# Performance work log

Hardware: AMD Instinct MI355X
Metric: run time of the kernel (lower is better)

## Reference

```python
import jax, jax.numpy as jnp
import numpy as np

N_NODES = 50000
N_EDGES = 800000
NEG_SLOPE = 0.2  # PyG GATConv default


def _glorot(key, shape):
    fan_in = shape[0] if len(shape) > 1 else shape[0]
    return jax.random.normal(key, shape, dtype=jnp.float32) / jnp.sqrt(jnp.float32(fan_in))


def setup_inputs() -> dict:
    key = jax.random.key(0)
    ks = jax.random.split(key, 12)
    x = jax.random.normal(ks[0], (N_NODES, 128), dtype=jnp.float32)
    edge_index = jax.random.randint(ks[1], (2, N_EDGES), 0, N_NODES, dtype=jnp.int64)
    return {
        "x": x,
        "edge_index": edge_index,
        # GAT layer 1: 128 -> 128 (heads=1)
        "W1": _glorot(ks[2], (128, 128)),
        "a_src1": _glorot(ks[3], (128,)),
        "a_dst1": _glorot(ks[4], (128,)),
        "b1": jnp.zeros((128,), dtype=jnp.float32),
        "Wres1": _glorot(ks[5], (128, 128)),
        # GAT layer 2: 128 -> 256
        "W2": _glorot(ks[6], (128, 256)),
        "a_src2": _glorot(ks[7], (256,)),
        "a_dst2": _glorot(ks[8], (256,)),
        "b2": jnp.zeros((256,), dtype=jnp.float32),
        "Wres2": _glorot(ks[9], (128, 256)),
    }


def _gat_layer(x, src, dst, W, a_src, a_dst, b, Wres, n):
    # h: [N, C_out] transformed node features
    h = x @ W
    # per-edge attention logit: gather scalar contributions, LeakyReLU
    logit = jax.nn.leaky_relu((h @ a_src)[src] + (h @ a_dst)[dst], NEG_SLOPE)  # [E]
    # numerically stable segment softmax over incoming edges of each dst node
    seg_max = jax.ops.segment_max(logit, dst, num_segments=n)  # [N]
    ex = jnp.exp(logit - seg_max[dst])
    denom = jax.ops.segment_sum(ex, dst, num_segments=n)  # [N]
    alpha = ex / denom[dst]  # [E]; self-loops guarantee denom > 0
    # weighted scatter-add aggregation
    out = jax.ops.segment_sum(alpha[:, None] * h[src], dst, num_segments=n)  # [N, C_out]
    # residual projection (in_dim != out_dim) + bias
    return out + x @ Wres + b


def reference(x, edge_index, W1, a_src1, a_dst1, b1, Wres1, W2, a_src2, a_dst2, b2, Wres2):
    n = x.shape[0]
    loops = jnp.arange(n, dtype=edge_index.dtype)  # add_self_loops=True (PyG default)
    src = jnp.concatenate([edge_index[0], loops])
    dst = jnp.concatenate([edge_index[1], loops])
    h = _gat_layer(x, src, dst, W1, a_src1, a_dst1, b1, Wres1, n)
    h = jax.nn.relu(h)
    return _gat_layer(h, src, dst, W2, a_src2, a_dst2, b2, Wres2, n)
```

## Files before the change

### kernel.cpp

```cpp
#include <hip/hip_runtime.h>
#include <math.h>

typedef __attribute__((ext_vector_type(8))) short bf16x8;
typedef __attribute__((ext_vector_type(4))) float f32x4;

__device__ inline unsigned short f2bf(float f) {
  union { float f; unsigned u; } x; x.f = f;
  unsigned r = x.u + 0x7FFF + ((x.u >> 16) & 1);
  return (unsigned short)(r >> 16);
}
__device__ inline float bf2f(unsigned short b) {
  union { unsigned u; float f; } x; x.u = ((unsigned)b) << 16;
  return x.f;
}


__global__ void convert_kernel(const void* edges, int E, int N,
                               int* __restrict__ src32, int* __restrict__ dst32,
                               int* __restrict__ counts) {
  int i = blockIdx.x * blockDim.x + threadIdx.x;
  int tot = E + N;
  if (i >= tot) return;
  int s, d;
  if (i < E) {
    const long long* q = (const long long*)edges;
    bool i64 = true;
#pragma unroll
    for (int k = 0; k < 8; ++k) {
      long long v = q[k];
      if (v < 0 || v >= (long long)N) i64 = false;
    }
    if (i64) {
      s = (int)q[i];
      d = (int)q[E + i];
    } else {
      s = ((const int*)edges)[i];
      d = ((const int*)edges)[E + i];
    }
  } else {
    s = d = i - E;
  }
  src32[i] = s;
  dst32[i] = d;
  atomicAdd(&counts[d], 1);
}


__global__ __launch_bounds__(256) void scan_partial(const int* __restrict__ counts,
                                                    int* __restrict__ bsum, int n) {
  int t = threadIdx.x;
  int base = blockIdx.x * 1024 + t * 4;
  int s = 0;
#pragma unroll
  for (int k = 0; k < 4; ++k) {
    int i = base + k;
    if (i < n) s += counts[i];
  }
#pragma unroll
  for (int off = 32; off; off >>= 1) s += __shfl_xor(s, off);
  __shared__ int red[4];
  if ((t & 63) == 0) red[t >> 6] = s;
  __syncthreads();
  if (t == 0) bsum[blockIdx.x] = red[0] + red[1] + red[2] + red[3];
}

__global__ __launch_bounds__(256) void scan_bsum(const int* __restrict__ bsum,
                                                 int* __restrict__ ebsum,
                                                 int* __restrict__ rowptr, int nblk, int n) {
  __shared__ int sh[256];
  int t = threadIdx.x;
  int v = (t < nblk) ? bsum[t] : 0;
  sh[t] = v;
  __syncthreads();
  for (int off = 1; off < 256; off <<= 1) {
    int u = (t >= off) ? sh[t - off] : 0;
    __syncthreads();
    sh[t] += u;
    __syncthreads();
  }
  if (t < nblk) ebsum[t] = sh[t] - v;
  if (t == nblk - 1) rowptr[n] = sh[t];
}

__global__ __launch_bounds__(256) void scan_final(const int* __restrict__ counts,
                                                  const int* __restrict__ ebsum,
                                                  int* __restrict__ rowptr,
                                                  int* __restrict__ cursor, int n) {
  int t = threadIdx.x;
  int lane = t & 63;
  int wv = t >> 6;
  int base = blockIdx.x * 1024 + t * 4;
  int c[4];
  int ts = 0;
#pragma unroll
  for (int k = 0; k < 4; ++k) {
    int i = base + k;
    c[k] = (i < n) ? counts[i] : 0;
    ts += c[k];
  }
  int ws = ts;
  for (int off = 1; off < 64; off <<= 1) {
    int u = __shfl_up(ws, off);
    if (lane >= off) ws += u;
  }
  __shared__ int wtot[4];
  if (lane == 63) wtot[wv] = ws;
  __syncthreads();
  int woff = 0;
  for (int k = 0; k < 4; ++k)
    if (k < wv) woff += wtot[k];
  int run = ebsum[blockIdx.x] + woff + (ws - ts);
#pragma unroll
  for (int k = 0; k < 4; ++k) {
    int i = base + k;
    if (i < n) {
      rowptr[i] = run;
      cursor[i] = run;
    }
    run += c[k];
  }
}

__global__ void scatter_kernel(const int* __restrict__ src32, const int* __restrict__ dst32,
                               int* __restrict__ cursor, int* __restrict__ csr_src, int tot) {
  int i = blockIdx.x * blockDim.x + threadIdx.x;
  if (i >= tot) return;
  int d = dst32[i];
  int slot = atomicAdd(&cursor[d], 1);
  csr_src[slot] = src32[i];
}


__global__ void cvt_all(const float* __restrict__ x,
                        const float* __restrict__ W1, const float* __restrict__ Wres1,
                        const float* __restrict__ W2, const float* __restrict__ Wres2,
                        unsigned short* __restrict__ x16,
                        unsigned short* __restrict__ w1t, unsigned short* __restrict__ wres1t,
                        unsigned short* __restrict__ w2t, unsigned short* __restrict__ wres2t,
                        int N, int Mpad) {
  int tid = blockIdx.x * blockDim.x + threadIdx.x;
  int xcnt = Mpad * 32;
  if (tid < xcnt) {
    int row = tid >> 5;
    int q = (tid & 31) << 2;
    unsigned short o0 = 0, o1 = 0, o2 = 0, o3 = 0;
    if (row < N) {
      float4 v = *(const float4*)(x + (size_t)row * 128 + q);
      o0 = f2bf(v.x); o1 = f2bf(v.y); o2 = f2bf(v.z); o3 = f2bf(v.w);
    }
    unsigned short* p = x16 + (size_t)row * 128 + q;
    p[0] = o0; p[1] = o1; p[2] = o2; p[3] = o3;
    return;
  }
  int t2 = tid - xcnt;
  const float* W;
  unsigned short* Wt;
  int C, loc;
  if (t2 < 16384) { W = W1; Wt = w1t; C = 128; loc = t2; }
  else if (t2 < 32768) { W = Wres1; Wt = wres1t; C = 128; loc = t2 - 16384; }
  else if (t2 < 65536) { W = W2; Wt = w2t; C = 256; loc = t2 - 32768; }
  else if (t2 < 98304) { W = Wres2; Wt = wres2t; C = 256; loc = t2 - 65536; }
  else return;
  int c = loc >> 7;
  int k = loc & 127;
  Wt[(size_t)c * 128 + k] = f2bf(W[(size_t)k * C + c]);
}


__global__ __launch_bounds__(256) void gemm_dual(
    const unsigned short* __restrict__ A,
    const unsigned short* __restrict__ Bh, const unsigned short* __restrict__ Br,
    unsigned short* __restrict__ Hout, unsigned short* __restrict__ Rout,
    const float* __restrict__ bias,
    const float* __restrict__ a_src, const float* __restrict__ a_dst,
    float* __restrict__ as_, float* __restrict__ ad_,
    int Nrows, int Ctot) {
  int l = threadIdx.x & 63;
  int w = threadIdx.x >> 6;
  int row_w = blockIdx.x * 128 + (w & 1) * 64;
  int col_w = blockIdx.y * 128 + (w >> 1) * 64;
  int lo = l & 15, hi = l >> 4;
  f32x4 ah[4][4], ar[4][4];
#pragma unroll
  for (int i = 0; i < 4; ++i)
#pragma unroll
    for (int j = 0; j < 4; ++j) {
      ah[i][j] = (f32x4){0.f, 0.f, 0.f, 0.f};
      ar[i][j] = (f32x4){0.f, 0.f, 0.f, 0.f};
    }

  const unsigned short* Ap = A + (size_t)(row_w + lo) * 128 + hi * 8;
  const unsigned short* Bhp = Bh + (size_t)(col_w + lo) * 128 + hi * 8;
  const unsigned short* Brp = Br + (size_t)(col_w + lo) * 128 + hi * 8;
#pragma unroll
  for (int kk = 0; kk < 4; ++kk) {
    bf16x8 a[4], bh[4], br[4];
#pragma unroll
    for (int f = 0; f < 4; ++f) {
      a[f] = *(const bf16x8*)(Ap + (size_t)f * 16 * 128 + kk * 32);
      bh[f] = *(const bf16x8*)(Bhp + (size_t)f * 16 * 128 + kk * 32);
      br[f] = *(const bf16x8*)(Brp + (size_t)f * 16 * 128 + kk * 32);
    }
#pragma unroll
    for (int fr = 0; fr < 4; ++fr)
#pragma unroll
      for (int fc = 0; fc < 4; ++fc) {
        ah[fr][fc] = __builtin_amdgcn_mfma_f32_16x16x32_bf16(a[fr], bh[fc], ah[fr][fc], 0, 0, 0);
        ar[fr][fc] = __builtin_amdgcn_mfma_f32_16x16x32_bf16(a[fr], br[fc], ar[fr][fc], 0, 0, 0);
      }
  }
  float wsrc[4], wdst[4], wb[4];
#pragma unroll
  for (int fc = 0; fc < 4; ++fc) {
    int col = col_w + fc * 16 + lo;
    wsrc[fc] = a_src[col];
    wdst[fc] = a_dst[col];
    wb[fc] = bias[col];
  }
#pragma unroll
  for (int fr = 0; fr < 4; ++fr) {
#pragma unroll
    for (int r = 0; r < 4; ++r) {
      int row = row_w + fr * 16 + hi * 4 + r;
      if (row < Nrows) {
        float s1 = 0.f, s2 = 0.f;
#pragma unroll
        for (int fc = 0; fc < 4; ++fc) {
          int col = col_w + fc * 16 + lo;
          float vh = ah[fr][fc][r];
          Hout[(size_t)row * Ctot + col] = f2bf(vh);
          s1 = fmaf(vh, wsrc[fc], s1);
          s2 = fmaf(vh, wdst[fc], s2);
          Rout[(size_t)row * Ctot + col] = f2bf(ar[fr][fc][r] + wb[fc]);
        }
#pragma unroll
        for (int off = 8; off; off >>= 1) {
          s1 += __shfl_xor(s1, off);
          s2 += __shfl_xor(s2, off);
        }
        if (lo == 0) {
          atomicAdd(&as_[row], s1);
          atomicAdd(&ad_[row], s2);
        }
      }
    }
  }
}


template <int C, bool L1>
__global__ __launch_bounds__(256) void aggregate_kernel(
    const unsigned short* __restrict__ h, unsigned short* __restrict__ res,
    float* __restrict__ outf,
    const float* __restrict__ as_, const float* __restrict__ ad_,
    const int* __restrict__ rowptr, const int* __restrict__ csr_src, int N) {
  const int FPL = C / 64;
  int wid = blockIdx.x * 4 + (threadIdx.x >> 6);
  int lane = threadIdx.x & 63;
  if (wid >= N) return;
  int base = rowptr[wid];
  int deg = rowptr[wid + 1] - base;
  float adn = ad_[wid];
  float m = -1e30f, ssum = 0.f;
  float acc[FPL];
#pragma unroll
  for (int c = 0; c < FPL; ++c) acc[c] = 0.f;
  for (int b0 = 0; b0 < deg; b0 += 64) {
    int idx = b0 + lane;
    int s = 0;
    float logit = -1e30f;
    if (idx < deg) {
      s = csr_src[base + idx];
      float tt = as_[s] + adn;
      logit = tt > 0.f ? tt : 0.2f * tt;
    }
    float cm = logit;
#pragma unroll
    for (int off = 32; off; off >>= 1) cm = fmaxf(cm, __shfl_xor(cm, off));
    float mnew = fmaxf(m, cm);
    float scale = __expf(m - mnew);
    ssum *= scale;
#pragma unroll
    for (int c = 0; c < FPL; ++c) acc[c] *= scale;
    float p = (idx < deg) ? __expf(logit - mnew) : 0.f;
    float ps = p;
#pragma unroll
    for (int off = 32; off; off >>= 1) ps += __shfl_xor(ps, off);
    ssum += ps;
    int cnt = min(64, deg - b0);
    int j = 0;
    for (; j + 8 <= cnt; j += 8) {
      float pj[8];
      int sj[8];
#pragma unroll
      for (int u = 0; u < 8; ++u) {
        pj[u] = __shfl(p, j + u);
        sj[u] = __shfl(s, j + u);
      }
      if (FPL == 2) {
        ushort2 v[8];
#pragma unroll
        for (int u = 0; u < 8; ++u)
          v[u] = *(const ushort2*)(h + (size_t)sj[u] * C + FPL * lane);
#pragma unroll
        for (int u = 0; u < 8; ++u) {
          acc[0] = fmaf(pj[u], bf2f(v[u].x), acc[0]);
          acc[1] = fmaf(pj[u], bf2f(v[u].y), acc[1]);
        }
      } else {
        ushort4 v[8];
#pragma unroll
        for (int u = 0; u < 8; ++u)
          v[u] = *(const ushort4*)(h + (size_t)sj[u] * C + FPL * lane);
#pragma unroll
        for (int u = 0; u < 8; ++u) {
          acc[0] = fmaf(pj[u], bf2f(v[u].x), acc[0]);
          acc[1] = fmaf(pj[u], bf2f(v[u].y), acc[1]);
          acc[2] = fmaf(pj[u], bf2f(v[u].z), acc[2]);
          acc[3] = fmaf(pj[u], bf2f(v[u].w), acc[3]);
        }
      }
    }
    for (; j < cnt; ++j) {
      float pj = __shfl(p, j);
      int sj = __shfl(s, j);
      const unsigned short* hs = h + (size_t)sj * C + FPL * lane;
      if (FPL == 2) {
        ushort2 hv = *(const ushort2*)hs;
        acc[0] = fmaf(pj, bf2f(hv.x), acc[0]);
        acc[1] = fmaf(pj, bf2f(hv.y), acc[1]);
      } else {
        ushort4 hv = *(const ushort4*)hs;
        acc[0] = fmaf(pj, bf2f(hv.x), acc[0]);
        acc[1] = fmaf(pj, bf2f(hv.y), acc[1]);
        acc[2] = fmaf(pj, bf2f(hv.z), acc[2]);
        acc[3] = fmaf(pj, bf2f(hv.w), acc[3]);
      }
    }
    m = mnew;
  }
  float inv = 1.f / ssum;
  size_t o = (size_t)wid * C + FPL * lane;
  if (L1) {
    unsigned short* p = res + o;
    ushort2 rv = *(const ushort2*)p;
    float v0 = fmaxf(acc[0] * inv + bf2f(rv.x), 0.f);
    float v1 = fmaxf(acc[1] * inv + bf2f(rv.y), 0.f);
    ushort2 ov; ov.x = f2bf(v0); ov.y = f2bf(v1);
    *(ushort2*)p = ov;
  } else {
    ushort4 rv = *(const ushort4*)(res + o);
    float4 ov;
    ov.x = acc[0] * inv + bf2f(rv.x);
    ov.y = acc[1] * inv + bf2f(rv.y);
    ov.z = acc[2] * inv + bf2f(rv.z);
    ov.w = acc[3] * inv + bf2f(rv.w);
    *(float4*)(outf + o) = ov;
  }
}


extern "C" void kernel_launch(void* const* d_in, const int* in_sizes, int n_in,
                              void* d_out, int out_size, void* d_ws, size_t ws_size,
                              hipStream_t stream) {
  const float* x = (const float*)d_in[0];
  const void* edges = d_in[1];
  const float* W1 = (const float*)d_in[2];
  const float* a_src1 = (const float*)d_in[3];
  const float* a_dst1 = (const float*)d_in[4];
  const float* b1 = (const float*)d_in[5];
  const float* Wres1 = (const float*)d_in[6];
  const float* W2 = (const float*)d_in[7];
  const float* a_src2 = (const float*)d_in[8];
  const float* a_dst2 = (const float*)d_in[9];
  const float* b2 = (const float*)d_in[10];
  const float* Wres2 = (const float*)d_in[11];
  float* out = (float*)d_out;

  int N = in_sizes[0] / 128;
  int E = in_sizes[1] / 2;
  int TOT = E + N;
  int Mpad = (N + 127) & ~127;
  int nblk = (N + 1023) >> 10;

  char* w = (char*)d_ws;
  size_t off = 0;
  auto alloc = [&](size_t bytes) {
    char* p = w + off;
    off += (bytes + 255) & ~(size_t)255;
    return p;
  };
  int* counts = (int*)alloc((size_t)N * 4);
  int* cursor = (int*)alloc((size_t)N * 4);
  int* rowptr = (int*)alloc((size_t)(N + 1) * 4);
  int* bsum = (int*)alloc(1024);
  int* ebsum = (int*)alloc(1024);
  float* as_ = (float*)alloc((size_t)N * 4);
  float* ad_ = (float*)alloc((size_t)N * 4);
  int* src32 = (int*)alloc((size_t)TOT * 4);
  int* dst32 = (int*)alloc((size_t)TOT * 4);
  int* csr = (int*)alloc((size_t)TOT * 4);
  unsigned short* x16 = (unsigned short*)alloc((size_t)Mpad * 128 * 2);
  unsigned short* w1t = (unsigned short*)alloc(128 * 128 * 2);
  unsigned short* wres1t = (unsigned short*)alloc(128 * 128 * 2);
  unsigned short* w2t = (unsigned short*)alloc(256 * 128 * 2);
  unsigned short* wres2t = (unsigned short*)alloc(256 * 128 * 2);
  unsigned short* h16 = (unsigned short*)alloc((size_t)N * 256 * 2);
  unsigned short* out1 = (unsigned short*)alloc((size_t)Mpad * 128 * 2);
  unsigned short* res2 = (unsigned short*)alloc((size_t)Mpad * 256 * 2);

  hipMemsetAsync(counts, 0, (size_t)N * 4, stream);
  hipMemsetAsync(out1 + (size_t)N * 128, 0, (size_t)(Mpad - N) * 128 * 2, stream);

  int gb = (TOT + 255) / 256;
  convert_kernel<<<gb, 256, 0, stream>>>(edges, E, N, src32, dst32, counts);
  scan_partial<<<nblk, 256, 0, stream>>>(counts, bsum, N);
  scan_bsum<<<1, 256, 0, stream>>>(bsum, ebsum, rowptr, nblk, N);
  scan_final<<<nblk, 256, 0, stream>>>(counts, ebsum, rowptr, cursor, N);
  scatter_kernel<<<gb, 256, 0, stream>>>(src32, dst32, cursor, csr, TOT);

  cvt_all<<<(Mpad * 32 + 98304 + 255) / 256, 256, 0, stream>>>(
      x, W1, Wres1, W2, Wres2, x16, w1t, wres1t, w2t, wres2t, N, Mpad);

  int mt = Mpad / 128;
  int sb = (N + 3) / 4;

  hipMemsetAsync(as_, 0, (size_t)N * 4, stream);
  hipMemsetAsync(ad_, 0, (size_t)N * 4, stream);
  gemm_dual<<<dim3(mt, 1), 256, 0, stream>>>(x16, w1t, wres1t, h16, out1, b1,
                                             a_src1, a_dst1, as_, ad_, N, 128);
  aggregate_kernel<128, true><<<sb, 256, 0, stream>>>(h16, out1, nullptr, as_, ad_, rowptr, csr, N);

  hipMemsetAsync(as_, 0, (size_t)N * 4, stream);
  hipMemsetAsync(ad_, 0, (size_t)N * 4, stream);
  gemm_dual<<<dim3(mt, 2), 256, 0, stream>>>(out1, w2t, wres2t, h16, res2, b2,
                                             a_src2, a_dst2, as_, ad_, N, 256);
  aggregate_kernel<256, false><<<sb, 256, 0, stream>>>(h16, res2, out, as_, ad_, rowptr, csr, N);
}
```

Baseline: 398.4 us.

## Split dual GEMM into two single-output kernels with swizzled LDS A tile

Replaces the fused dual-output GEMM (which kept two 4x4 accumulator sets per wave) with a templated single-output GEMM launched twice, once for the attention projection and once for the residual projection. The A tile is staged into shared memory with an XOR swizzle so the two column-warps share it instead of each reloading from global. This halves accumulator register pressure, which may raise occupancy. In exchange, A is read from global twice across the two launches and there is an extra kernel launch per layer.

```diff
diff --git a/kernel.cpp b/kernel.cpp
--- a/kernel.cpp
+++ b/kernel.cpp
@@ -167,55 +167,69 @@
 }
 
 
-__global__ __launch_bounds__(256) void gemm_dual(
+template <int SCAL>
+__global__ __launch_bounds__(256) void gemm_tile(
     const unsigned short* __restrict__ A,
-    const unsigned short* __restrict__ Bh, const unsigned short* __restrict__ Br,
-    unsigned short* __restrict__ Hout, unsigned short* __restrict__ Rout,
+    const unsigned short* __restrict__ Bt,
+    unsigned short* __restrict__ Cout,
     const float* __restrict__ bias,
     const float* __restrict__ a_src, const float* __restrict__ a_dst,
     float* __restrict__ as_, float* __restrict__ ad_,
     int Nrows, int Ctot) {
-  int l = threadIdx.x & 63;
-  int w = threadIdx.x >> 6;
-  int row_w = blockIdx.x * 128 + (w & 1) * 64;
+  __shared__ unsigned short Asw[128 * 128];
+  int t = threadIdx.x;
+  int row0 = blockIdx.x * 128;
+
+#pragma unroll
+  for (int i = 0; i < 8; ++i) {
+    int li = i * 256 + t;
+    int r = li >> 4;
+    int c = li & 15;
+    bf16x8 v = *(const bf16x8*)(A + (size_t)(row0 + r) * 128 + c * 8);
+    *(bf16x8*)(Asw + r * 128 + ((c ^ (r & 7)) * 8)) = v;
+  }
+  __syncthreads();
+
+  int w = t >> 6;
+  int l = t & 63;
+  int lo = l & 15, hi = l >> 4;
+  int row_w = row0 + (w & 1) * 64;
   int col_w = blockIdx.y * 128 + (w >> 1) * 64;
-  int lo = l & 15, hi = l >> 4;
-  f32x4 ah[4][4], ar[4][4];
+  int rt0 = (w & 1) * 64 + lo;
+
+  f32x4 acc[4][4];
 #pragma unroll
   for (int i = 0; i < 4; ++i)
 #pragma unroll
-    for (int j = 0; j < 4; ++j) {
-      ah[i][j] = (f32x4){0.f, 0.f, 0.f, 0.f};
-      ar[i][j] = (f32x4){0.f, 0.f, 0.f, 0.f};
-    }
-
-  const unsigned short* Ap = A + (size_t)(row_w + lo) * 128 + hi * 8;
-  const unsigned short* Bhp = Bh + (size_t)(col_w + lo) * 128 + hi * 8;
-  const unsigned short* Brp = Br + (size_t)(col_w + lo) * 128 + hi * 8;
+    for (int j = 0; j < 4; ++j) acc[i][j] = (f32x4){0.f, 0.f, 0.f, 0.f};
+
+  const unsigned short* Bp = Bt + (size_t)(col_w + lo) * 128 + hi * 8;
 #pragma unroll
   for (int kk = 0; kk < 4; ++kk) {
-    bf16x8 a[4], bh[4], br[4];
+    int blk = (kk * 4 + hi) ^ (lo & 7);
+    bf16x8 a[4], b[4];
 #pragma unroll
     for (int f = 0; f < 4; ++f) {
-      a[f] = *(const bf16x8*)(Ap + (size_t)f * 16 * 128 + kk * 32);
-      bh[f] = *(const bf16x8*)(Bhp + (size_t)f * 16 * 128 + kk * 32);
-      br[f] = *(const bf16x8*)(Brp + (size_t)f * 16 * 128 + kk * 32);
+      a[f] = *(const bf16x8*)(Asw + (rt0 + f * 16) * 128 + blk * 8);
+      b[f] = *(const bf16x8*)(Bp + (size_t)f * 16 * 128 + kk * 32);
     }
 #pragma unroll
     for (int fr = 0; fr < 4; ++fr)
 #pragma unroll
-      for (int fc = 0; fc < 4; ++fc) {
-        ah[fr][fc] = __builtin_amdgcn_mfma_f32_16x16x32_bf16(a[fr], bh[fc], ah[fr][fc], 0, 0, 0);
-        ar[fr][fc] = __builtin_amdgcn_mfma_f32_16x16x32_bf16(a[fr], br[fc], ar[fr][fc], 0, 0, 0);
-      }
-  }
-  float wsrc[4], wdst[4], wb[4];
+      for (int fc = 0; fc < 4; ++fc)
+        acc[fr][fc] = __builtin_amdgcn_mfma_f32_16x16x32_bf16(a[fr], b[fc], acc[fr][fc], 0, 0, 0);
+  }
+
+  float w0[4], w1[4];
 #pragma unroll
   for (int fc = 0; fc < 4; ++fc) {
     int col = col_w + fc * 16 + lo;
-    wsrc[fc] = a_src[col];
-    wdst[fc] = a_dst[col];
-    wb[fc] = bias[col];
+    if (SCAL) {
+      w0[fc] = a_src[col];
+      w1[fc] = a_dst[col];
+    } else {
+      w0[fc] = bias[col];
+    }
   }
 #pragma unroll
   for (int fr = 0; fr < 4; ++fr) {
@@ -227,20 +241,25 @@
 #pragma unroll
         for (int fc = 0; fc < 4; ++fc) {
           int col = col_w + fc * 16 + lo;
-          float vh = ah[fr][fc][r];
-          Hout[(size_t)row * Ctot + col] = f2bf(vh);
-          s1 = fmaf(vh, wsrc[fc], s1);
-          s2 = fmaf(vh, wdst[fc], s2);
-          Rout[(size_t)row * Ctot + col] = f2bf(ar[fr][fc][r] + wb[fc]);
+          float v = acc[fr][fc][r];
+          if (SCAL) {
+            s1 = fmaf(v, w0[fc], s1);
+            s2 = fmaf(v, w1[fc], s2);
+          } else {
+            v += w0[fc];
+          }
+          Cout[(size_t)row * Ctot + col] = f2bf(v);
         }
-#pragma unroll
-        for (int off = 8; off; off >>= 1) {
-          s1 += __shfl_xor(s1, off);
-          s2 += __shfl_xor(s2, off);
-        }
-        if (lo == 0) {
-          atomicAdd(&as_[row], s1);
-          atomicAdd(&ad_[row], s2);
+        if (SCAL) {
+#pragma unroll
+          for (int off = 8; off; off >>= 1) {
+            s1 += __shfl_xor(s1, off);
+            s2 += __shfl_xor(s2, off);
+          }
+          if (lo == 0) {
+            atomicAdd(&as_[row], s1);
+            atomicAdd(&ad_[row], s2);
+          }
         }
       }
     }
@@ -427,13 +446,17 @@
 
   hipMemsetAsync(as_, 0, (size_t)N * 4, stream);
   hipMemsetAsync(ad_, 0, (size_t)N * 4, stream);
-  gemm_dual<<<dim3(mt, 1), 256, 0, stream>>>(x16, w1t, wres1t, h16, out1, b1,
-                                             a_src1, a_dst1, as_, ad_, N, 128);
+  gemm_tile<1><<<dim3(mt, 1), 256, 0, stream>>>(x16, w1t, h16, nullptr,
+                                                a_src1, a_dst1, as_, ad_, N, 128);
+  gemm_tile<0><<<dim3(mt, 1), 256, 0, stream>>>(x16, wres1t, out1, b1,
+                                                nullptr, nullptr, nullptr, nullptr, N, 128);
   aggregate_kernel<128, true><<<sb, 256, 0, stream>>>(h16, out1, nullptr, as_, ad_, rowptr, csr, N);
 
   hipMemsetAsync(as_, 0, (size_t)N * 4, stream);
   hipMemsetAsync(ad_, 0, (size_t)N * 4, stream);
-  gemm_dual<<<dim3(mt, 2), 256, 0, stream>>>(out1, w2t, wres2t, h16, res2, b2,
-                                             a_src2, a_dst2, as_, ad_, N, 256);
+  gemm_tile<1><<<dim3(mt, 2), 256, 0, stream>>>(out1, w2t, h16, nullptr,
+                                                a_src2, a_dst2, as_, ad_, N, 256);
+  gemm_tile<0><<<dim3(mt, 2), 256, 0, stream>>>(out1, wres2t, res2, b2,
+                                                nullptr, nullptr, nullptr, nullptr, N, 256);
   aggregate_kernel<256, false><<<sb, 256, 0, stream>>>(h16, res2, out, as_, ad_, rowptr, csr, N);
 }
```

New measurement: 382.9 us. -3.9%, faster.
